# Performance work log

Hardware: AMD Instinct MI355X
Metric: run time of the kernel (lower is better)

## Reference

```python
import jax, jax.numpy as jnp
import numpy as np

B, IN_LEN, H, OUT_LEN = 256, 512, 512, 10


def _gru_cell(x, h, w_ih, w_hh, b_ih, b_hh):
    # x: [B, D_in], h: [B, H]; PyTorch GRU gate order: r, z, n
    gi = x @ w_ih.T + b_ih          # [B, 3H]
    gh = h @ w_hh.T + b_hh          # [B, 3H]
    i_r, i_z, i_n = jnp.split(gi, 3, axis=-1)
    h_r, h_z, h_n = jnp.split(gh, 3, axis=-1)
    r = jax.nn.sigmoid(i_r + h_r)
    z = jax.nn.sigmoid(i_z + h_z)
    n = jnp.tanh(i_n + r * h_n)
    return (1.0 - z) * n + z * h


def _gru_layer(xs, h0, w_ih, w_hh, b_ih, b_hh):
    # xs: [T, B, D_in] -> outputs [T, B, H], final h [B, H]
    def step(h, x):
        h_new = _gru_cell(x, h, w_ih, w_hh, b_ih, b_hh)
        return h_new, h_new
    h_T, ys = jax.lax.scan(step, h0, xs)
    return ys, h_T


def setup_inputs() -> dict:
    key = jax.random.key(0)
    ks = jax.random.split(key, 24)
    s = 1.0 / np.sqrt(H)
    def u(k, shape):
        return jax.random.uniform(k, shape, jnp.float32, -s, s)
    inp = {"x": jax.random.normal(ks[0], (B, IN_LEN, 2), jnp.float32)}
    # encoder layer 0 (input_dim=2), layer 1 (input H)
    inp["enc_w_ih0"] = u(ks[1], (3 * H, 2)); inp["enc_w_hh0"] = u(ks[2], (3 * H, H))
    inp["enc_b_ih0"] = u(ks[3], (3 * H,));  inp["enc_b_hh0"] = u(ks[4], (3 * H,))
    inp["enc_w_ih1"] = u(ks[5], (3 * H, H)); inp["enc_w_hh1"] = u(ks[6], (3 * H, H))
    inp["enc_b_ih1"] = u(ks[7], (3 * H,));  inp["enc_b_hh1"] = u(ks[8], (3 * H,))
    inp["ln_gamma"] = jnp.ones((H,), jnp.float32)
    inp["ln_beta"] = jnp.zeros((H,), jnp.float32)
    # decoder layer 0 (input_dim=1), layer 1
    inp["dec_w_ih0"] = u(ks[9], (3 * H, 1));  inp["dec_w_hh0"] = u(ks[10], (3 * H, H))
    inp["dec_b_ih0"] = u(ks[11], (3 * H,));   inp["dec_b_hh0"] = u(ks[12], (3 * H,))
    inp["dec_w_ih1"] = u(ks[13], (3 * H, H)); inp["dec_w_hh1"] = u(ks[14], (3 * H, H))
    inp["dec_b_ih1"] = u(ks[15], (3 * H,));   inp["dec_b_hh1"] = u(ks[16], (3 * H,))
    inp["fc_w"] = u(ks[17], (1, H)); inp["fc_b"] = u(ks[18], (1,))
    return inp


def reference(x,
              enc_w_ih0, enc_w_hh0, enc_b_ih0, enc_b_hh0,
              enc_w_ih1, enc_w_hh1, enc_b_ih1, enc_b_hh1,
              ln_gamma, ln_beta,
              dec_w_ih0, dec_w_hh0, dec_b_ih0, dec_b_hh0,
              dec_w_ih1, dec_w_hh1, dec_b_ih1, dec_b_hh1,
              fc_w, fc_b):
    b = x.shape[0]
    h0 = jnp.zeros((b, H), x.dtype)
    xs = jnp.swapaxes(x, 0, 1)                      # [T, B, 2]
    ys0, hT0 = _gru_layer(xs, h0, enc_w_ih0, enc_w_hh0, enc_b_ih0, enc_b_hh0)
    _, hT1 = _gru_layer(ys0, h0, enc_w_ih1, enc_w_hh1, enc_b_ih1, enc_b_hh1)
    # LayerNorm over hidden dim of stacked h [2, B, H]
    def ln(v):
        mu = jnp.mean(v, axis=-1, keepdims=True)
        var = jnp.var(v, axis=-1, keepdims=True)
        return (v - mu) / jnp.sqrt(var + 1e-5) * ln_gamma + ln_beta
    h_dec0, h_dec1 = ln(hT0), ln(hT1)
    dec_in = x[:, -1, 1:2]                          # [B, 1]

    def dec_step(carry, _):
        h0c, h1c, inp = carry
        h0n = _gru_cell(inp, h0c, dec_w_ih0, dec_w_hh0, dec_b_ih0, dec_b_hh0)
        h1n = _gru_cell(h0n, h1c, dec_w_ih1, dec_w_hh1, dec_b_ih1, dec_b_hh1)
        y = h1n @ fc_w.T + fc_b                     # [B, 1]
        return (h0n, h1n, y), y

    _, outs = jax.lax.scan(dec_step, (h_dec0, h_dec1, dec_in), None, length=OUT_LEN)
    return jnp.swapaxes(outs, 0, 1)                 # [B, out_len, 1]
```

## Files before the change

kernel.cpp:

```cpp
#include <hip/hip_runtime.h>
#include <math.h>


#define Hdim 512
#define Bsz  256
#define Tlen 512
#define OUTL 10

typedef _Float16 half8 __attribute__((ext_vector_type(8)));
typedef float    f32x4 __attribute__((ext_vector_type(4)));
typedef unsigned long long u64;

__device__ __forceinline__ f32x4 mfma16(half8 a, half8 b, f32x4 c) {
    return __builtin_amdgcn_mfma_f32_16x16x32_f16(a, b, c, 0, 0, 0);
}
__device__ __forceinline__ float sigf(float v) { return 1.0f / (1.0f + __expf(-v)); }
__device__ __forceinline__ half8 h8(u64 lo, u64 hi) {
    union { u64 u[2]; half8 h; } t; t.u[0] = lo; t.u[1] = hi; return t.h;
}

__device__ __forceinline__ u64 a_ld8(const void* p) {
    return __hip_atomic_load((const u64*)p, __ATOMIC_RELAXED, __HIP_MEMORY_SCOPE_AGENT); }
__device__ __forceinline__ float a_ld4(const void* p) {
    return __hip_atomic_load((const float*)p, __ATOMIC_RELAXED, __HIP_MEMORY_SCOPE_AGENT); }
__device__ __forceinline__ int a_ldi(const int* p) {
    return __hip_atomic_load(p, __ATOMIC_RELAXED, __HIP_MEMORY_SCOPE_AGENT); }
__device__ __forceinline__ void a_st8(void* p, u64 v) {
    __hip_atomic_store((u64*)p, v, __ATOMIC_RELAXED, __HIP_MEMORY_SCOPE_AGENT); }
__device__ __forceinline__ void a_st4(void* p, float v) {
    __hip_atomic_store((float*)p, v, __ATOMIC_RELAXED, __HIP_MEMORY_SCOPE_AGENT); }
__device__ __forceinline__ void a_st2(void* p, unsigned short v) {
    __hip_atomic_store((unsigned short*)p, v, __ATOMIC_RELAXED, __HIP_MEMORY_SCOPE_AGENT); }
__device__ __forceinline__ void a_sti(int* p, int v) {
    __hip_atomic_store(p, v, __ATOMIC_RELAXED, __HIP_MEMORY_SCOPE_AGENT); }

__device__ __forceinline__ void sigS(int* slot, int val) {
    asm volatile("s_waitcnt vmcnt(0)" ::: "memory");
    if ((threadIdx.x & 63) == 0) a_sti(slot, val);
}
template <int NS>
__device__ __forceinline__ void waitS(int* base, int target) {
    if (target <= 0) return;
    int* p = base + ((threadIdx.x & 63) % NS);
    while (true) {
        int v = a_ldi(p);
        if (__all(v >= target)) break;
        __builtin_amdgcn_s_sleep(1);
    }
    asm volatile("" ::: "memory");
}

__device__ __forceinline__ half8 ld_cvt(const float* p) {
    float4 a = *(const float4*)p;
    float4 b = *(const float4*)(p + 4);
    half8 v;
    v[0]=(_Float16)a.x; v[1]=(_Float16)a.y; v[2]=(_Float16)a.z; v[3]=(_Float16)a.w;
    v[4]=(_Float16)b.x; v[5]=(_Float16)b.y; v[6]=(_Float16)b.z; v[7]=(_Float16)b.w;
    return v;
}

__device__ void ln_rows(float* hT, _Float16* dst16rg, const float* gam, const float* bet,
                        int row0, int lane) {
    #pragma unroll 1
    for (int r = 0; r < 16; ++r) {
        float* pr_ = hT + (size_t)(row0 + r) * Hdim;
        float v[8];
        #pragma unroll
        for (int e = 0; e < 4; ++e) {
            union { u64 u; float f[2]; } c;
            c.u = a_ld8(pr_ + lane * 8 + e * 2);
            v[2*e] = c.f[0]; v[2*e+1] = c.f[1];
        }
        float s = 0.f, sq = 0.f;
        #pragma unroll
        for (int e = 0; e < 8; ++e) { s += v[e]; sq += v[e] * v[e]; }
        #pragma unroll
        for (int m = 1; m < 64; m <<= 1) { s += __shfl_xor(s, m); sq += __shfl_xor(sq, m); }
        float mean = s * (1.0f / Hdim);
        float rstd = rsqrtf(sq * (1.0f / Hdim) - mean * mean + 1e-5f);
        _Float16* d = dst16rg + (lane >> 1) * 256 + r * 16 + (lane & 1) * 8;
        #pragma unroll
        for (int e = 0; e < 8; ++e) {
            int k = lane * 8 + e;
            float o = (v[e] - mean) * rstd * gam[k] + bet[k];
            a_st4(pr_ + k, o);
            a_st2(d + e, __builtin_bit_cast(unsigned short, (_Float16)o));
        }
    }
}

#define OFF_FLAGS 0
#define SZ_FLAGS  (6 * 16 * 32 * 4)
#define H16B      262144
#define OFF_H0R   (OFF_FLAGS + SZ_FLAGS)
#define OFF_H1R   (OFF_H0R + 4 * H16B)
#define ZBYTES    (OFF_H1R + 2 * H16B)
#define OFF_H0D   ZBYTES
#define OFF_H1D   (OFF_H0D + 2 * H16B)
#define OFF_HT0   (OFF_H1D + 2 * H16B)
#define OFF_HT1   (OFF_HT0 + 524288)
#define OFF_YB    (OFF_HT1 + 524288)
#define WS_NEED   (OFF_YB + 1024)

__global__ __launch_bounds__(512, 1) void gru_all(
    const float* __restrict__ x,
    const float* __restrict__ ewih0, const float* __restrict__ ewhh0,
    const float* __restrict__ ebih0, const float* __restrict__ ebhh0,
    const float* __restrict__ ewih1, const float* __restrict__ ewhh1,
    const float* __restrict__ ebih1, const float* __restrict__ ebhh1,
    const float* __restrict__ lng,   const float* __restrict__ lnb,
    const float* __restrict__ dwih0, const float* __restrict__ dwhh0,
    const float* __restrict__ dbih0, const float* __restrict__ dbhh0,
    const float* __restrict__ dwih1, const float* __restrict__ dwhh1,
    const float* __restrict__ dbih1, const float* __restrict__ dbhh1,
    const float* __restrict__ fcw,   const float* __restrict__ fcb,
    float* __restrict__ out, char* __restrict__ ws)
{
    __shared__ _Float16 ldsY[8192];
    __shared__ _Float16 ldsH[8192];
    __shared__ float    ldsAcc[4][3][272];
    __shared__ _Float16 ldsOut[8][256];

    const int tid  = threadIdx.x;
    const int wid  = tid >> 6, lane = tid & 63;
    const int rg   = blockIdx.x & 15;
    const int g    = blockIdx.x >> 4;
    const bool poolA = (g < 4);
    const int cv   = lane & 15, kg = lane >> 4;
    const int row0 = rg * 16;
    const int rb   = kg * 4;
    const size_t rgbase = (size_t)rg * 32 * 256;

    int* flags = (int*)(ws + OFF_FLAGS);
    int* f0  = flags + (0 * 16 + rg) * 32;
    int* f1  = flags + (1 * 16 + rg) * 32;
    int* fD0 = flags + (2 * 16 + rg) * 32;
    int* fD1 = flags + (3 * 16 + rg) * 32;
    int* fLN = flags + (4 * 16 + rg) * 32;
    int* fY  = flags + (5 * 16 + rg) * 32;
    _Float16* h0r[4] = {(_Float16*)(ws+OFF_H0R), (_Float16*)(ws+OFF_H0R+H16B),
                        (_Float16*)(ws+OFF_H0R+2*H16B), (_Float16*)(ws+OFF_H0R+3*H16B)};
    _Float16* h1r[2] = {(_Float16*)(ws+OFF_H1R), (_Float16*)(ws+OFF_H1R+H16B)};
    _Float16* h0d[2] = {(_Float16*)(ws+OFF_H0D), (_Float16*)(ws+OFF_H0D+H16B)};
    _Float16* h1d[2] = {(_Float16*)(ws+OFF_H1D), (_Float16*)(ws+OFF_H1D+H16B)};
    float* hT0  = (float*)(ws + OFF_HT0);
    float* hT1  = (float*)(ws + OFF_HT1);
    float* ybuf = (float*)(ws + OFF_YB);

    const bool gi = (!poolA) && (wid < 4);
    const int  hs = poolA ? (g * 8 + wid) : ((g - 4) * 4 + (wid & 3));
    const int  hid = hs * 16 + cv;
    const int  ow = poolA ? wid : (wid & 3);

#define LDS_A(ARR, KK) \
    (*(const half8*)&(ARR)[(2 * (KK) + (kg >> 1)) * 256 + cv * 16 + (kg & 1) * 8])
#define STORE_TILE(DST, HV0, HV1, HV2, HV3)                                      \
    do {                                                                         \
        ldsOut[ow][(rb + 0) * 16 + cv] = (_Float16)(HV0);                        \
        ldsOut[ow][(rb + 1) * 16 + cv] = (_Float16)(HV1);                        \
        ldsOut[ow][(rb + 2) * 16 + cv] = (_Float16)(HV2);                        \
        ldsOut[ow][(rb + 3) * 16 + cv] = (_Float16)(HV3);                        \
        u64 pk_ = *(const u64*)&ldsOut[ow][lane * 4];                            \
        a_st8((DST) + rgbase + (size_t)hs * 256 + lane * 4, pk_);                \
    } while (0)

    half8 w0[16], w1[16], w2[16];
    {
        const float* wsP = poolA ? ewhh0 : (gi ? ewih1 : ewhh1);
        const float* b0 = wsP + (size_t)hid * Hdim + kg * 8;
        #pragma unroll
        for (int kk = 0; kk < 16; ++kk) {
            w0[kk] = ld_cvt(b0 + kk * 32);
            w1[kk] = ld_cvt(b0 + (size_t)512 * Hdim + kk * 32);
            w2[kk] = ld_cvt(b0 + (size_t)1024 * Hdim + kk * 32);
        }
    }
    float cw_r0 = 0, cw_r1 = 0, cw_z0 = 0, cw_z1 = 0, cw_n0 = 0, cw_n1 = 0;
    float bCr = 0, bCz = 0, bIn = 0, bHn = 0;
    if (poolA) {
        cw_r0 = ewih0[hid * 2];          cw_r1 = ewih0[hid * 2 + 1];
        cw_z0 = ewih0[(512 + hid) * 2];  cw_z1 = ewih0[(512 + hid) * 2 + 1];
        cw_n0 = ewih0[(1024 + hid) * 2]; cw_n1 = ewih0[(1024 + hid) * 2 + 1];
        bCr = ebih0[hid] + ebhh0[hid];
        bCz = ebih0[512 + hid] + ebhh0[512 + hid];
        bIn = ebih0[1024 + hid]; bHn = ebhh0[1024 + hid];
    } else if (!gi) {
        bCr = ebih1[hid] + ebhh1[hid];
        bCz = ebih1[512 + hid] + ebhh1[512 + hid];
        bIn = ebih1[1024 + hid]; bHn = ebhh1[1024 + hid];
    }
    float hold[4] = {0.f, 0.f, 0.f, 0.f};

    if (poolA) {
        for (int i = 0; i < Tlen; ++i) {
            float2 xv[4];
            #pragma unroll
            for (int jj = 0; jj < 4; ++jj)
                xv[jj] = *(const float2*)(x + ((size_t)(row0 + rb + jj) * Tlen + i) * 2);
            waitS<32>(f1, i - 3);
            waitS<32>(f0, i);
            {
                const _Float16* s = h0r[(i + 3) & 3] + rgbase;
                u64 tv[4];
                #pragma unroll
                for (int u = 0; u < 4; ++u) tv[u] = a_ld8(s + (tid + u * 512) * 4);
                #pragma unroll
                for (int u = 0; u < 4; ++u) *(u64*)&ldsY[(tid + u * 512) * 4] = tv[u];
            }
            __syncthreads();
            f32x4 a0 = {0,0,0,0}, a1 = {0,0,0,0}, a2 = {0,0,0,0};
            #pragma unroll
            for (int kk = 0; kk < 16; ++kk) {
                half8 a = LDS_A(ldsY, kk);
                a0 = mfma16(a, w0[kk], a0);
                a1 = mfma16(a, w1[kk], a1);
                a2 = mfma16(a, w2[kk], a2);
            }
            float hv[4];
            #pragma unroll
            for (int jj = 0; jj < 4; ++jj) {
                int b = row0 + rb + jj;
                float x0 = xv[jj].x, x1 = xv[jj].y;
                float r = sigf(x0 * cw_r0 + x1 * cw_r1 + a0[jj] + bCr);
                float z = sigf(x0 * cw_z0 + x1 * cw_z1 + a1[jj] + bCz);
                float n = tanhf(x0 * cw_n0 + x1 * cw_n1 + bIn + r * (a2[jj] + bHn));
                hv[jj] = (1.0f - z) * n + z * hold[jj];
                hold[jj] = hv[jj];
                if (i == Tlen - 1) a_st4(hT0 + (size_t)b * Hdim + hid, hv[jj]);
            }
            STORE_TILE(h0r[i & 3], hv[0], hv[1], hv[2], hv[3]);
            sigS(f0 + hs, i + 1);
        }
    } else {
        for (int u = 0; u < Tlen; ++u) {
            waitS<32>(f1, u);
            waitS<32>(f0, u + 1);
            {
                const _Float16* sy = h0r[u & 3] + rgbase;
                const _Float16* sh = h1r[(u + 1) & 1] + rgbase;
                u64 ty[4], th[4];
                #pragma unroll
                for (int v = 0; v < 4; ++v) {
                    ty[v] = a_ld8(sy + (tid + v * 512) * 4);
                    th[v] = a_ld8(sh + (tid + v * 512) * 4);
                }
                #pragma unroll
                for (int v = 0; v < 4; ++v) {
                    *(u64*)&ldsY[(tid + v * 512) * 4] = ty[v];
                    *(u64*)&ldsH[(tid + v * 512) * 4] = th[v];
                }
            }
            __syncthreads();
            f32x4 a0 = {0,0,0,0}, a1 = {0,0,0,0}, a2 = {0,0,0,0};
            if (gi) {
                #pragma unroll
                for (int kk = 0; kk < 16; ++kk) {
                    half8 a = LDS_A(ldsY, kk);
                    a0 = mfma16(a, w0[kk], a0);
                    a1 = mfma16(a, w1[kk], a1);
                    a2 = mfma16(a, w2[kk], a2);
                }
                #pragma unroll
                for (int jj = 0; jj < 4; ++jj) {
                    int rr = (rb + jj) * 17 + cv;
                    ldsAcc[wid][0][rr] = a0[jj];
                    ldsAcc[wid][1][rr] = a1[jj];
                    ldsAcc[wid][2][rr] = a2[jj];
                }
            } else {
                #pragma unroll
                for (int kk = 0; kk < 16; ++kk) {
                    half8 a = LDS_A(ldsH, kk);
                    a0 = mfma16(a, w0[kk], a0);
                    a1 = mfma16(a, w1[kk], a1);
                    a2 = mfma16(a, w2[kk], a2);
                }
            }
            __syncthreads();
            if (!gi) {
                float hv[4];
                #pragma unroll
                for (int jj = 0; jj < 4; ++jj) {
                    int b = row0 + rb + jj;
                    int rr = (rb + jj) * 17 + cv;
                    float gr = ldsAcc[wid & 3][0][rr];
                    float gz = ldsAcc[wid & 3][1][rr];
                    float gn = ldsAcc[wid & 3][2][rr];
                    float r = sigf(gr + a0[jj] + bCr);
                    float z = sigf(gz + a1[jj] + bCz);
                    float n = tanhf(gn + bIn + r * (a2[jj] + bHn));
                    hv[jj] = (1.0f - z) * n + z * hold[jj];
                    hold[jj] = hv[jj];
                    if (u == Tlen - 1) a_st4(hT1 + (size_t)b * Hdim + hid, hv[jj]);
                }
                STORE_TILE(h1r[u & 1], hv[0], hv[1], hv[2], hv[3]);
                sigS(f1 + hs, u + 1);
            }
        }
    }

    if (poolA && g == 0 && wid == 0) {
        waitS<32>(f0, Tlen);
        ln_rows(hT0, h0d[1] + rgbase, lng, lnb, row0, lane);
        if (lane < 16) {
            int b = row0 + lane;
            a_st4(ybuf + b, x[((size_t)b * Tlen + (Tlen - 1)) * 2 + 1]);
        }
        sigS(fLN + 0, 1);
    }
    if (!poolA && g == 4 && wid == 0) {
        waitS<32>(f1, Tlen);
        ln_rows(hT1, h1d[1] + rgbase, lng, lnb, row0, lane);
        sigS(fLN + 1, 1);
    }

    {
        const float* wsP = poolA ? dwhh0 : (gi ? dwih1 : dwhh1);
        const float* b0 = wsP + (size_t)hid * Hdim + kg * 8;
        #pragma unroll
        for (int kk = 0; kk < 16; ++kk) {
            w0[kk] = ld_cvt(b0 + kk * 32);
            w1[kk] = ld_cvt(b0 + (size_t)512 * Hdim + kk * 32);
            w2[kk] = ld_cvt(b0 + (size_t)1024 * Hdim + kk * 32);
        }
    }
    if (poolA) {
        cw_r0 = dwih0[hid]; cw_z0 = dwih0[512 + hid]; cw_n0 = dwih0[1024 + hid];
        bCr = dbih0[hid] + dbhh0[hid];
        bCz = dbih0[512 + hid] + dbhh0[512 + hid];
        bIn = dbih0[1024 + hid]; bHn = dbhh0[1024 + hid];
    } else if (!gi) {
        bCr = dbih1[hid] + dbhh1[hid];
        bCz = dbih1[512 + hid] + dbhh1[512 + hid];
        bIn = dbih1[1024 + hid]; bHn = dbhh1[1024 + hid];
    }
    float fw[8] = {0,0,0,0,0,0,0,0};
    float fb = 0.f;
    const bool is_fc = (!poolA) && (g == 4) && (wid == 7);
    if (is_fc) {
        #pragma unroll
        for (int e = 0; e < 8; ++e) fw[e] = fcw[lane * 8 + e];
        fb = fcb[0];
    }
    waitS<2>(fLN, 1);
    if (poolA) {
        #pragma unroll
        for (int jj = 0; jj < 4; ++jj)
            hold[jj] = a_ld4(hT0 + (size_t)(row0 + rb + jj) * Hdim + hid);
    } else if (!gi) {
        #pragma unroll
        for (int jj = 0; jj < 4; ++jj)
            hold[jj] = a_ld4(hT1 + (size_t)(row0 + rb + jj) * Hdim + hid);
    }

    if (poolA) {
        for (int t = 0; t < OUTL; ++t) {
            waitS<32>(fD0, t);
            waitS<1>(fY, t);
            {
                const _Float16* s = h0d[(t + 1) & 1] + rgbase;
                u64 tv[4];
                #pragma unroll
                for (int u = 0; u < 4; ++u) tv[u] = a_ld8(s + (tid + u * 512) * 4);
                #pragma unroll
                for (int u = 0; u < 4; ++u) *(u64*)&ldsY[(tid + u * 512) * 4] = tv[u];
            }
            __syncthreads();
            float yvv[4];
            #pragma unroll
            for (int jj = 0; jj < 4; ++jj) yvv[jj] = a_ld4(ybuf + row0 + rb + jj);
            f32x4 a0 = {0,0,0,0}, a1 = {0,0,0,0}, a2 = {0,0,0,0};
            #pragma unroll
            for (int kk = 0; kk < 16; ++kk) {
                half8 a = LDS_A(ldsY, kk);
                a0 = mfma16(a, w0[kk], a0);
                a1 = mfma16(a, w1[kk], a1);
                a2 = mfma16(a, w2[kk], a2);
            }
            float hv[4];
            #pragma unroll
            for (int jj = 0; jj < 4; ++jj) {
                float yv = yvv[jj];
                float r = sigf(yv * cw_r0 + a0[jj] + bCr);
                float z = sigf(yv * cw_z0 + a1[jj] + bCz);
                float n = tanhf(yv * cw_n0 + bIn + r * (a2[jj] + bHn));
                hv[jj] = (1.0f - z) * n + z * hold[jj];
                hold[jj] = hv[jj];
            }
            STORE_TILE(h0d[t & 1], hv[0], hv[1], hv[2], hv[3]);
            sigS(fD0 + hs, t + 1);
        }
    } else {
        for (int t = 0; t < OUTL; ++t) {
            waitS<32>(fD1, t);
            {
                const _Float16* s = h1d[(t + 1) & 1] + rgbase;
                u64 tv[4];
                #pragma unroll
                for (int u = 0; u < 4; ++u) tv[u] = a_ld8(s + (tid + u * 512) * 4);
                #pragma unroll
                for (int u = 0; u < 4; ++u) *(u64*)&ldsH[(tid + u * 512) * 4] = tv[u];
            }
            __syncthreads();
            f32x4 a0 = {0,0,0,0}, a1 = {0,0,0,0}, a2 = {0,0,0,0};
            if (gi) {
                waitS<32>(fD0, t + 1);
                const _Float16* agb = h0d[t & 1] + rgbase;
                #pragma unroll
                for (int kk = 0; kk < 16; ++kk) {
                    const _Float16* pa = agb + (2 * kk + (kg >> 1)) * 256
                                       + cv * 16 + (kg & 1) * 8;
                    half8 q = h8(a_ld8(pa), a_ld8(pa + 4));
                    a0 = mfma16(q, w0[kk], a0);
                    a1 = mfma16(q, w1[kk], a1);
                    a2 = mfma16(q, w2[kk], a2);
                }
                #pragma unroll
                for (int jj = 0; jj < 4; ++jj) {
                    int rr = (rb + jj) * 17 + cv;
                    ldsAcc[wid][0][rr] = a0[jj];
                    ldsAcc[wid][1][rr] = a1[jj];
                    ldsAcc[wid][2][rr] = a2[jj];
                }
            } else {
                #pragma unroll
                for (int kk = 0; kk < 16; ++kk) {
                    half8 a = LDS_A(ldsH, kk);
                    a0 = mfma16(a, w0[kk], a0);
                    a1 = mfma16(a, w1[kk], a1);
                    a2 = mfma16(a, w2[kk], a2);
                }
            }
            __syncthreads();
            if (!gi) {
                float hv[4];
                #pragma unroll
                for (int jj = 0; jj < 4; ++jj) {
                    int rr = (rb + jj) * 17 + cv;
                    float gr = ldsAcc[wid & 3][0][rr];
                    float gz = ldsAcc[wid & 3][1][rr];
                    float gn = ldsAcc[wid & 3][2][rr];
                    float r = sigf(gr + a0[jj] + bCr);
                    float z = sigf(gz + a1[jj] + bCz);
                    float n = tanhf(gn + bIn + r * (a2[jj] + bHn));
                    hv[jj] = (1.0f - z) * n + z * hold[jj];
                    hold[jj] = hv[jj];
                }
                STORE_TILE(h1d[t & 1], hv[0], hv[1], hv[2], hv[3]);
                sigS(fD1 + hs, t + 1);
                if (is_fc) {
                    waitS<32>(fD1, t + 1);
                    const _Float16* hb = h1d[t & 1] + rgbase;
                    #pragma unroll 1
                    for (int r2 = 0; r2 < 16; ++r2) {
                        const _Float16* hp8 = hb + (lane >> 1) * 256 + r2 * 16 + (lane & 1) * 8;
                        half8 hv8 = h8(a_ld8(hp8), a_ld8(hp8 + 4));
                        float pa = 0.f;
                        #pragma unroll
                        for (int e = 0; e < 8; ++e) pa += (float)hv8[e] * fw[e];
                        #pragma unroll
                        for (int m = 1; m < 64; m <<= 1) pa += __shfl_xor(pa, m);
                        if (lane == 0) {
                            int b = row0 + r2;
                            float yv2 = pa + fb;
                            a_st4(ybuf + b, yv2);
                            out[(size_t)b * OUTL + t] = yv2;
                        }
                    }
                    sigS(fY, t + 1);
                }
            }
        }
    }
#undef STORE_TILE
#undef LDS_A
}

extern "C" void kernel_launch(void* const* d_in, const int* in_sizes, int n_in,
                              void* d_out, int out_size, void* d_ws, size_t ws_size,
                              hipStream_t stream)
{
    (void)in_sizes; (void)n_in; (void)out_size; (void)ws_size;
    hipMemsetAsync(d_ws, 0, ZBYTES, stream);
    gru_all<<<192, 512, 0, stream>>>(
        (const float*)d_in[0],
        (const float*)d_in[1],  (const float*)d_in[2],
        (const float*)d_in[3],  (const float*)d_in[4],
        (const float*)d_in[5],  (const float*)d_in[6],
        (const float*)d_in[7],  (const float*)d_in[8],
        (const float*)d_in[9],  (const float*)d_in[10],
        (const float*)d_in[11], (const float*)d_in[12],
        (const float*)d_in[13], (const float*)d_in[14],
        (const float*)d_in[15], (const float*)d_in[16],
        (const float*)d_in[17], (const float*)d_in[18],
        (const float*)d_in[19], (const float*)d_in[20],
        (float*)d_out, (char*)d_ws);
}
```

Before: 4.240 ms.

## Replace per-step flag handshakes with sequence-tagged data words in encoder exchange

The encoder's inter-block hidden-state exchange now packs a step sequence number into the upper 32 bits of each 64-bit store, next to 32 bits of fp16 data. Consumers poll the data itself until every word carries the expected tag, which removes the separate per-step flag waits and the store-then-signal ordering. A consumer counter (cons0) lets pool A hold off overwriting a ring slot until pool B has read it, and the layer-1 buffer becomes a 4-deep ring. The cost is twice the bytes moved per exchange and spin-polling on data words, with correctness depending on each tagged 64-bit store being seen atomically.

```diff
diff --git a/kernel.cpp b/kernel.cpp
--- a/kernel.cpp
+++ b/kernel.cpp
@@ -10,6 +10,7 @@
 typedef _Float16 half8 __attribute__((ext_vector_type(8)));
 typedef float    f32x4 __attribute__((ext_vector_type(4)));
 typedef unsigned long long u64;
+typedef unsigned int uint;
 
 __device__ __forceinline__ f32x4 mfma16(half8 a, half8 b, f32x4 c) {
     return __builtin_amdgcn_mfma_f32_16x16x32_f16(a, b, c, 0, 0, 0);
@@ -90,17 +91,18 @@
 }
 
 #define OFF_FLAGS 0
-#define SZ_FLAGS  (6 * 16 * 32 * 4)
+#define SZ_FLAGS  (8 * 16 * 32 * 4)
+#define RUNITS    4096
+#define RSLOTSZ   (16 * RUNITS * 8)
+#define OFF_H0R   (OFF_FLAGS + SZ_FLAGS)
+#define OFF_H1R   (OFF_H0R + 4 * RSLOTSZ)
+#define ZBYTES    (OFF_H1R + 4 * RSLOTSZ)
 #define H16B      262144
-#define OFF_H0R   (OFF_FLAGS + SZ_FLAGS)
-#define OFF_H1R   (OFF_H0R + 4 * H16B)
-#define ZBYTES    (OFF_H1R + 2 * H16B)
 #define OFF_H0D   ZBYTES
 #define OFF_H1D   (OFF_H0D + 2 * H16B)
 #define OFF_HT0   (OFF_H1D + 2 * H16B)
 #define OFF_HT1   (OFF_HT0 + 524288)
 #define OFF_YB    (OFF_HT1 + 524288)
-#define WS_NEED   (OFF_YB + 1024)
 
 __global__ __launch_bounds__(512, 1) void gru_all(
     const float* __restrict__ x,
@@ -132,15 +134,16 @@
     const size_t rgbase = (size_t)rg * 32 * 256;
 
     int* flags = (int*)(ws + OFF_FLAGS);
-    int* f0  = flags + (0 * 16 + rg) * 32;
-    int* f1  = flags + (1 * 16 + rg) * 32;
-    int* fD0 = flags + (2 * 16 + rg) * 32;
-    int* fD1 = flags + (3 * 16 + rg) * 32;
-    int* fLN = flags + (4 * 16 + rg) * 32;
-    int* fY  = flags + (5 * 16 + rg) * 32;
-    _Float16* h0r[4] = {(_Float16*)(ws+OFF_H0R), (_Float16*)(ws+OFF_H0R+H16B),
-                        (_Float16*)(ws+OFF_H0R+2*H16B), (_Float16*)(ws+OFF_H0R+3*H16B)};
-    _Float16* h1r[2] = {(_Float16*)(ws+OFF_H1R), (_Float16*)(ws+OFF_H1R+H16B)};
+    int* fEnc0 = flags + (0 * 16 + rg) * 32;
+    int* fEnc1 = flags + (1 * 16 + rg) * 32;
+    int* fD0   = flags + (2 * 16 + rg) * 32;
+    int* fD1   = flags + (3 * 16 + rg) * 32;
+    int* fLN   = flags + (4 * 16 + rg) * 32;
+    int* fY    = flags + (5 * 16 + rg) * 32;
+    int* cons0 = flags + (6 * 16 + rg) * 32;
+
+    u64* r0rg = (u64*)(ws + OFF_H0R) + (size_t)rg * RUNITS;
+    u64* r1rg = (u64*)(ws + OFF_H1R) + (size_t)rg * RUNITS;
     _Float16* h0d[2] = {(_Float16*)(ws+OFF_H0D), (_Float16*)(ws+OFF_H0D+H16B)};
     _Float16* h1d[2] = {(_Float16*)(ws+OFF_H1D), (_Float16*)(ws+OFF_H1D+H16B)};
     float* hT0  = (float*)(ws + OFF_HT0);
@@ -154,6 +157,19 @@
 
 #define LDS_A(ARR, KK) \
     (*(const half8*)&(ARR)[(2 * (KK) + (kg >> 1)) * 256 + cv * 16 + (kg & 1) * 8])
+#define STORE_SEQ(DSTSLOT, SEQ, HV0, HV1, HV2, HV3)                              \
+    do {                                                                         \
+        ldsOut[ow][(rb + 0) * 16 + cv] = (_Float16)(HV0);                        \
+        ldsOut[ow][(rb + 1) * 16 + cv] = (_Float16)(HV1);                        \
+        ldsOut[ow][(rb + 2) * 16 + cv] = (_Float16)(HV2);                        \
+        ldsOut[ow][(rb + 3) * 16 + cv] = (_Float16)(HV3);                        \
+        uint d0_ = ((uint*)&ldsOut[ow][0])[lane * 2];                            \
+        uint d1_ = ((uint*)&ldsOut[ow][0])[lane * 2 + 1];                        \
+        u64* dst_ = (DSTSLOT) + hs * 128 + lane * 2;                             \
+        u64 sq_ = ((u64)(uint)(SEQ)) << 32;                                      \
+        a_st8(dst_,     sq_ | d0_);                                              \
+        a_st8(dst_ + 1, sq_ | d1_);                                              \
+    } while (0)
 #define STORE_TILE(DST, HV0, HV1, HV2, HV3)                                      \
     do {                                                                         \
         ldsOut[ow][(rb + 0) * 16 + cv] = (_Float16)(HV0);                        \
@@ -197,16 +213,21 @@
             #pragma unroll
             for (int jj = 0; jj < 4; ++jj)
                 xv[jj] = *(const float2*)(x + ((size_t)(row0 + rb + jj) * Tlen + i) * 2);
-            waitS<32>(f1, i - 3);
-            waitS<32>(f0, i);
-            {
-                const _Float16* s = h0r[(i + 3) & 3] + rgbase;
-                u64 tv[4];
-                #pragma unroll
-                for (int u = 0; u < 4; ++u) tv[u] = a_ld8(s + (tid + u * 512) * 4);
-                #pragma unroll
-                for (int u = 0; u < 4; ++u) *(u64*)&ldsY[(tid + u * 512) * 4] = tv[u];
-            }
+            const u64* src = r0rg + (size_t)((i + 3) & 3) * (16 * RUNITS);
+            const uint tgt = (uint)i;
+            u64 v[8];
+            #pragma unroll
+            for (int k = 0; k < 8; ++k) v[k] = a_ld8(src + tid + k * 512);
+            while (true) {
+                bool all = true;
+                #pragma unroll
+                for (int k = 0; k < 8; ++k)
+                    if ((uint)(v[k] >> 32) != tgt) { all = false; v[k] = a_ld8(src + tid + k * 512); }
+                if (all) break;
+                __builtin_amdgcn_s_sleep(1);
+            }
+            #pragma unroll
+            for (int k = 0; k < 8; ++k) ((uint*)ldsY)[tid + k * 512] = (uint)v[k];
             __syncthreads();
             f32x4 a0 = {0,0,0,0}, a1 = {0,0,0,0}, a2 = {0,0,0,0};
             #pragma unroll
@@ -228,29 +249,39 @@
                 hold[jj] = hv[jj];
                 if (i == Tlen - 1) a_st4(hT0 + (size_t)b * Hdim + hid, hv[jj]);
             }
-            STORE_TILE(h0r[i & 3], hv[0], hv[1], hv[2], hv[3]);
-            sigS(f0 + hs, i + 1);
-        }
+            waitS<8>(cons0, i - 3);
+            STORE_SEQ(r0rg + (size_t)(i & 3) * (16 * RUNITS), i + 1,
+                      hv[0], hv[1], hv[2], hv[3]);
+        }
+        sigS(fEnc0 + hs, 1);
     } else {
         for (int u = 0; u < Tlen; ++u) {
-            waitS<32>(f1, u);
-            waitS<32>(f0, u + 1);
-            {
-                const _Float16* sy = h0r[u & 3] + rgbase;
-                const _Float16* sh = h1r[(u + 1) & 1] + rgbase;
-                u64 ty[4], th[4];
-                #pragma unroll
-                for (int v = 0; v < 4; ++v) {
-                    ty[v] = a_ld8(sy + (tid + v * 512) * 4);
-                    th[v] = a_ld8(sh + (tid + v * 512) * 4);
-                }
-                #pragma unroll
-                for (int v = 0; v < 4; ++v) {
-                    *(u64*)&ldsY[(tid + v * 512) * 4] = ty[v];
-                    *(u64*)&ldsH[(tid + v * 512) * 4] = th[v];
-                }
+            const u64* sy = r0rg + (size_t)(u & 3) * (16 * RUNITS);
+            const u64* sh = r1rg + (size_t)((u + 3) & 3) * (16 * RUNITS);
+            const uint ty = (uint)(u + 1), th = (uint)u;
+            u64 vy[8], vh[8];
+            #pragma unroll
+            for (int k = 0; k < 8; ++k) {
+                vy[k] = a_ld8(sy + tid + k * 512);
+                vh[k] = a_ld8(sh + tid + k * 512);
+            }
+            while (true) {
+                bool all = true;
+                #pragma unroll
+                for (int k = 0; k < 8; ++k) {
+                    if ((uint)(vy[k] >> 32) != ty) { all = false; vy[k] = a_ld8(sy + tid + k * 512); }
+                    if ((uint)(vh[k] >> 32) != th) { all = false; vh[k] = a_ld8(sh + tid + k * 512); }
+                }
+                if (all) break;
+                __builtin_amdgcn_s_sleep(1);
+            }
+            #pragma unroll
+            for (int k = 0; k < 8; ++k) {
+                ((uint*)ldsY)[tid + k * 512] = (uint)vy[k];
+                ((uint*)ldsH)[tid + k * 512] = (uint)vh[k];
             }
             __syncthreads();
+            if (tid == 0) a_sti(cons0 + (g - 4), u + 1);
             f32x4 a0 = {0,0,0,0}, a1 = {0,0,0,0}, a2 = {0,0,0,0};
             if (gi) {
                 #pragma unroll
@@ -293,14 +324,15 @@
                     hold[jj] = hv[jj];
                     if (u == Tlen - 1) a_st4(hT1 + (size_t)b * Hdim + hid, hv[jj]);
                 }
-                STORE_TILE(h1r[u & 1], hv[0], hv[1], hv[2], hv[3]);
-                sigS(f1 + hs, u + 1);
-            }
-        }
+                STORE_SEQ(r1rg + (size_t)(u & 3) * (16 * RUNITS), u + 1,
+                          hv[0], hv[1], hv[2], hv[3]);
+            }
+        }
+        if (!gi) sigS(fEnc1 + hs, 1);
     }
 
     if (poolA && g == 0 && wid == 0) {
-        waitS<32>(f0, Tlen);
+        waitS<32>(fEnc0, 1);
         ln_rows(hT0, h0d[1] + rgbase, lng, lnb, row0, lane);
         if (lane < 16) {
             int b = row0 + lane;
@@ -309,7 +341,7 @@
         sigS(fLN + 0, 1);
     }
     if (!poolA && g == 4 && wid == 0) {
-        waitS<32>(f1, Tlen);
+        waitS<32>(fEnc1, 1);
         ln_rows(hT1, h1d[1] + rgbase, lng, lnb, row0, lane);
         sigS(fLN + 1, 1);
     }
@@ -472,6 +504,7 @@
             }
         }
     }
+#undef STORE_SEQ
 #undef STORE_TILE
 #undef LDS_A
 }
```

New measurement: 4.202 ms. About the same (-0.9%).
